# Optimization experiments

Measured on AMD Instinct MI355X. Metric: run time of the kernel, lower is better.

Reference implementation:

```python
import jax, jax.numpy as jnp
import numpy as np

# ---- static config (mirrors YOLOLayer init kwargs) ----
ANCHORS_ALL = jnp.array([[10.,13.],[16.,30.],[33.,23.],[30.,61.],[62.,45.],
                         [59.,119.],[116.,90.],[156.,198.],[373.,326.]], jnp.float32)
MASK = jnp.array([0, 1, 2], jnp.int32)
ANCHORS_PX = ANCHORS_ALL[:3]          # this scale's anchors, pixels
NUM_CLASSES = 1                       # forced by p_boxes.view(..., 6) in _first_loss
IMG_W = IMG_H = 608.0
B, A, GH, GW = 32, 3, 76, 76          # stride-8 head of a 608x608 YOLOv3
T = 48                                # number of ground-truth boxes
IGNORE_THRES = 0.5                    # ignore_thres_first_loss


def _bce(p, t):
    # torch BCELoss clamps log terms at -100
    return -(t * jnp.clip(jnp.log(p), -100.0) + (1.0 - t) * jnp.clip(jnp.log(1.0 - p), -100.0))


def _xywh2xyxy(b):
    xy, wh = b[..., :2], b[..., 2:4]
    return jnp.concatenate([xy - wh / 2, xy + wh / 2], -1)


def setup_inputs() -> dict:
    key = jax.random.key(0)
    k1, k2, k3 = jax.random.split(key, 3)
    x = jax.random.normal(k1, (B, A * (5 + NUM_CLASSES), GH, GW), jnp.float32) * 0.5
    # targets: [image_idx, cx, cy, w, h, cls], normalized coords; ids sorted, first = 0
    img_ids = jnp.sort(jnp.arange(T) % B).astype(jnp.float32)
    xy = jax.random.uniform(k2, (T, 2), minval=0.05, maxval=0.95)
    wh = jax.random.uniform(k3, (T, 2), minval=0.02, maxval=0.30)
    cls = jnp.zeros((T, 1), jnp.float32)
    target = jnp.concatenate([img_ids[:, None], xy, wh, cls], axis=1)
    return {"x": x, "target": target}


def _forward(x, target):
    stride_w, stride_h = IMG_W / GW, IMG_H / GH
    scale_anchors = ANCHORS_PX / jnp.array([stride_w, stride_h], jnp.float32)  # grid units

    pred = x.reshape(B, A, 5 + NUM_CLASSES, GH, GW).transpose(0, 1, 3, 4, 2)   # [B,A,H,W,5+C]
    cx = jax.nn.sigmoid(pred[..., 0]); cy = jax.nn.sigmoid(pred[..., 1])
    pw = pred[..., 2]; ph = pred[..., 3]
    pconf = jax.nn.sigmoid(pred[..., 4]); pcls = jax.nn.sigmoid(pred[..., 5:])

    # ---- __detect: decode boxes to pixel coords ----
    bx = cx + jnp.arange(GW, dtype=jnp.float32)[None, None, None, :]
    by = cy + jnp.arange(GH, dtype=jnp.float32)[None, None, :, None]
    bw = jnp.exp(pw) * scale_anchors[:, 0][None, :, None, None]
    bh = jnp.exp(ph) * scale_anchors[:, 1][None, :, None, None]
    boxes_px = jnp.stack([bx * stride_w, by * stride_h, bw * stride_w, bh * stride_h], -1).reshape(B, -1, 4)
    output = jnp.concatenate([boxes_px, pconf.reshape(B, -1, 1), pcls.reshape(B, -1, NUM_CLASSES)], -1)

    # ---- _first_loss: ignore mask from IoU(decoded preds, GT) in normalized coords ----
    timg = (target[:, 0] - target[0, 0]).astype(jnp.int32)                 # [T]
    tb = target[:, 1:5]                                                    # normalized xywh
    pbn = jnp.stack([bx / GW, by / GH, bw / GW, bh / GH], -1).reshape(B, -1, 4)  # [B,M,4]
    tc = _xywh2xyxy(tb)[:, None, None, :]                                  # [T,1,1,4]
    pc = _xywh2xyxy(pbn)[None]                                             # [1,B,M,4]
    iw = jnp.clip(jnp.minimum(tc[..., 2], pc[..., 2]) - jnp.maximum(tc[..., 0], pc[..., 0]), 0.0)
    ih = jnp.clip(jnp.minimum(tc[..., 3], pc[..., 3]) - jnp.maximum(tc[..., 1], pc[..., 1]), 0.0)
    inter = iw * ih
    ta = (tb[:, 2] * tb[:, 3])[:, None, None]
    pa = (pbn[..., 2] * pbn[..., 3])[None]
    iou = inter / (ta + pa - inter + 1e-16)                                # [T,B,M]
    match = timg[:, None] == jnp.arange(B)[None, :]                        # [T,B] GT-to-image
    best = jnp.max(jnp.where(match[:, :, None], iou, -1.0), 0)             # [B,M]
    ignore_mask = (best <= IGNORE_THRES).astype(jnp.float32).reshape(B, A, GH, GW)

    # ---- __build_target ----
    gxy = tb[:, :2] * jnp.array([GW, GH], jnp.float32)
    gwh = tb[:, 2:4] * jnp.array([GW, GH], jnp.float32)
    gwh_n = tb[:, 2:4]
    label = target[:, 5].astype(jnp.int32)
    an = ANCHORS_ALL / jnp.array([IMG_W, IMG_H], jnp.float32)              # [9,2] normalized
    w_inter = jnp.minimum(an[:, 0:1], gwh_n[None, :, 0]) * jnp.minimum(an[:, 1:2], gwh_n[None, :, 1])
    w_union = (an[:, 0] * an[:, 1] + 1e-16)[:, None] + (gwh_n[:, 0] * gwh_n[:, 1])[None, :] - w_inter
    anc_iou = w_inter / w_union                                            # [9,T]
    best_idx = jnp.argmax(anc_iou, 0)                                      # [T]
    gi = gxy[:, 0].astype(jnp.int32); gj = gxy[:, 1].astype(jnp.int32)
    in_mask = jnp.any(best_idx[:, None] == MASK[None, :], 1)
    valid = in_mask & (gi < GW) & (gj < GH) & (gi >= 0) & (gj >= 0)
    bi = best_idx - MASK[0]
    sc = 2.0 - gwh_n[:, 0] * gwh_n[:, 1]
    img_s = jnp.where(valid, timg, B)          # invalid rows -> OOB batch idx, dropped by scatter
    idx = (img_s, bi, gj, gi)

    z = jnp.zeros((B, A, GH, GW), jnp.float32)
    obj = z.at[idx].set(1.0, mode='drop')
    noobj = jnp.ones((B, A, GH, GW), jnp.float32).at[idx].set(0.0, mode='drop')
    tx = z.at[idx].set(gxy[:, 0] - jnp.floor(gxy[:, 0]), mode='drop')
    ty = z.at[idx].set(gxy[:, 1] - jnp.floor(gxy[:, 1]), mode='drop')
    tw = z.at[idx].set(jnp.log(gwh[:, 0] * stride_w / ANCHORS_PX[bi, 0] + 1e-16), mode='drop')
    th = z.at[idx].set(jnp.log(gwh[:, 1] * stride_h / ANCHORS_PX[bi, 1] + 1e-16), mode='drop')
    tconf = obj
    tcls = jnp.zeros((B, A, GH, GW, NUM_CLASSES), jnp.float32).at[img_s, bi, gj, gi, label].set(1.0, mode='drop')
    scale = jnp.ones((B, A, GH, GW), jnp.float32).at[idx].set(sc, mode='drop')

    # ignore_mask[obj==1] = 1 ; noobj_mask[ignore_mask==0] = 0
    ignore = jnp.where(obj > 0, 1.0, ignore_mask)
    noobj = jnp.where(ignore == 0, 0.0, noobj)

    s2 = scale * scale
    loss_x = jnp.sum(obj * (cx - tx) ** 2 * s2)
    loss_y = jnp.sum(obj * (cy - ty) ** 2 * s2)
    loss_w = jnp.sum(obj * (pw - tw) ** 2 * s2)
    loss_h = jnp.sum(obj * (ph - th) ** 2 * s2)
    loss_conf_obj = jnp.sum(obj * _bce(pconf, tconf))
    loss_conf_noobj = jnp.sum(noobj * _bce(pconf, tconf))
    loss_cls = jnp.sum(obj[..., None] * _bce(pcls, tcls))
    loss_conf = loss_conf_obj + loss_conf_noobj
    total = loss_x + loss_y + loss_w + loss_h + loss_conf + loss_cls
    r = lambda v: jnp.reshape(v, (1,))
    return (output, r(total), r(loss_x + loss_y), r(loss_w + loss_h), r(loss_conf), r(loss_cls))


def reference(x, target):
    return _forward(x, target)
```

## Files before the change

### kernel.cpp

```cpp
#include <hip/hip_runtime.h>

#define NB 32
#define NA 3
#define NGH 76
#define NGW 76
#define NT 48
#define PLANE (NGH * NGW)
#define NCELL (NB * NA * PLANE)
#define NOUT  (NCELL * 6)
#define CPT 2
#define BLK 256
#define NTHREAD (NCELL / CPT)
#define NBLKS (NTHREAD / BLK)
#define MAGIC 0x59A10C47u

static_assert(NTHREAD % BLK == 0, "grid must divide evenly");
static_assert(5 * BLK >= NBLKS, "poll covers all flags in one unrolled pass");


__launch_bounds__(BLK, 6)
__global__ void yolo_main(const float* __restrict__ x,
                          const float* __restrict__ tgt,
                          float* __restrict__ out,
                          float* __restrict__ partials,
                          unsigned int* __restrict__ flags,
                          float* __restrict__ lossbuf) {
    __shared__ float st[NT * 16];
    __shared__ unsigned long long sball[NB];
    __shared__ int soff[NB + 1];
    __shared__ int sord[NT];
    __shared__ float red[4][4];

    const int tx  = threadIdx.x;
    const int bid = blockIdx.x;
    const int tid = bid * BLK + tx;
    const int g   = tid * CPT;

    const int gw0 = g % NGW;
    const int gh  = (g / NGW) % NGH;
    const int a   = (g / PLANE) % NA;
    const int b   = g / (NA * PLANE);

    const float* xp = x + (size_t)(b * (NA * 6) + a * 6) * PLANE + (g % PLANE);
    const float2 v0 = *(const float2*)(xp);
    const float2 v1 = *(const float2*)(xp + PLANE);
    const float2 v2 = *(const float2*)(xp + 2 * PLANE);
    const float2 v3 = *(const float2*)(xp + 3 * PLANE);
    const float2 v4 = *(const float2*)(xp + 4 * PLANE);
    const float2 v5 = *(const float2*)(xp + 5 * PLANE);

    if (tx < 64) {
        const int t = tx;
        const bool isT = (t < NT);
        int timg = 999;
        if (isT) {
            const float t00 = tgt[0];
            const float* tr = tgt + t * 6;
            timg = (int)(tr[0] - t00);
            const float bxn = tr[1], byn = tr[2], bwn = tr[3], bhn = tr[4];

            const float gx = bxn * (float)NGW;
            const float gy = byn * (float)NGH;
            const int gi = (int)gx;
            const int gj = (int)gy;
            const float tarea = bwn * bhn;

            const float aw_px[9] = {10.f,16.f,33.f,30.f,62.f,59.f,116.f,156.f,373.f};
            const float ah_px[9] = {13.f,30.f,23.f,61.f,45.f,119.f,90.f,198.f,326.f};
            int bidx = 0; float biou = -1e30f;
            #pragma unroll
            for (int k = 0; k < 9; ++k) {
                const float aw = aw_px[k] / 608.0f;
                const float ah = ah_px[k] / 608.0f;
                const float wi = fminf(aw, bwn) * fminf(ah, bhn);
                const float un = ((aw * ah + 1e-16f) + tarea) - wi;
                const float iou = wi / un;
                if (iou > biou) { biou = iou; bidx = k; }
            }
            const bool inm = (bidx >= 0) && (bidx <= 2);
            const bool valid = inm && (gi < NGW) && (gj < NGH) && (gi >= 0) && (gj >= 0);
            const int bic = bidx < 0 ? 0 : (bidx > 2 ? 2 : bidx);
            const float apw = (bic == 0) ? 10.f : ((bic == 1) ? 16.f : 33.f);
            const float aph = (bic == 0) ? 13.f : ((bic == 1) ? 30.f : 23.f);

            float* s = st + t * 16;
            s[0]  = (float)timg;
            s[1]  = valid ? 1.0f : 0.0f;
            s[2]  = (float)bidx;
            s[3]  = (float)gj;
            s[4]  = (float)gi;
            s[5]  = gx - floorf(gx);
            s[6]  = gy - floorf(gy);
            s[7]  = __logf(((bwn * (float)NGW) * 8.0f) / apw + 1e-16f);
            s[8]  = __logf(((bhn * (float)NGH) * 8.0f) / aph + 1e-16f);
            s[9]  = 2.0f - bwn * bhn;
            s[10] = bxn - bwn * 0.5f;
            s[11] = byn - bhn * 0.5f;
            s[12] = bxn + bwn * 0.5f;
            s[13] = byn + bhn * 0.5f;
            s[14] = tarea;
            s[15] = 0.0f;
        }

        int cnt = 0;
        for (int bb = 0; bb < NB; ++bb) {
            const unsigned long long m = __ballot(timg == bb);
            if (t == 0) sball[bb] = m;
            if (t == bb) cnt = (int)__popcll(m);
        }
        int inc = cnt;
        #pragma unroll
        for (int d = 1; d < 32; d <<= 1) {
            const int v = __shfl_up(inc, d);
            if (t >= d) inc += v;
        }
        if (t < NB) soff[t] = inc - cnt;
        if (t == NB - 1) soff[NB] = inc;
        if (isT) {
            const unsigned long long m = sball[timg];
            const int rank = (int)__popcll(m & ((1ULL << t) - 1ULL));
            sord[soff[timg] + rank] = t;
        }
    }

    const float p0[CPT] = {v0.x, v0.y};
    const float p1[CPT] = {v1.x, v1.y};
    const float p2[CPT] = {v2.x, v2.y};
    const float p3[CPT] = {v3.x, v3.y};
    const float p4[CPT] = {v4.x, v4.y};
    const float p5[CPT] = {v5.x, v5.y};

    const float sa_w = (a == 0) ? 1.25f  : ((a == 1) ? 2.0f  : 4.125f);
    const float sa_h = (a == 0) ? 1.625f : ((a == 1) ? 3.75f : 2.875f);

    float cxv[CPT], cyv[CPT], pcf[CPT], pcl[CPT];
    float px1[CPT], py1[CPT], px2[CPT], py2[CPT], par[CPT];
    float o12[CPT * 6];

    #pragma unroll
    for (int c = 0; c < CPT; ++c) {
        const float cx    = 1.0f / (1.0f + __expf(-p0[c]));
        const float cy    = 1.0f / (1.0f + __expf(-p1[c]));
        const float pconf = 1.0f / (1.0f + __expf(-p4[c]));
        const float pcls  = 1.0f / (1.0f + __expf(-p5[c]));
        const float bx = cx + (float)(gw0 + c);
        const float by = cy + (float)gh;
        const float bw = __expf(p2[c]) * sa_w;
        const float bh = __expf(p3[c]) * sa_h;

        o12[c * 6 + 0] = bx * 8.0f;
        o12[c * 6 + 1] = by * 8.0f;
        o12[c * 6 + 2] = bw * 8.0f;
        o12[c * 6 + 3] = bh * 8.0f;
        o12[c * 6 + 4] = pconf;
        o12[c * 6 + 5] = pcls;

        const float pxc = bx * (1.0f / NGW), pyc = by * (1.0f / NGH);
        const float pwn = bw * (1.0f / NGW), phn = bh * (1.0f / NGH);
        cxv[c] = cx; cyv[c] = cy; pcf[c] = pconf; pcl[c] = pcls;
        px1[c] = pxc - pwn * 0.5f; py1[c] = pyc - phn * 0.5f;
        px2[c] = pxc + pwn * 0.5f; py2[c] = pyc + phn * 0.5f;
        par[c] = pwn * phn;
    }

    {
        float4* ob = (float4*)(out + (size_t)g * 6);
        ob[0] = make_float4(o12[0], o12[1], o12[2],  o12[3]);
        ob[1] = make_float4(o12[4], o12[5], o12[6],  o12[7]);
        ob[2] = make_float4(o12[8], o12[9], o12[10], o12[11]);
    }

    __syncthreads();

    float best[CPT] = {-1.f, -1.f};
    int   so[CPT]   = {-1, -1};
    {
        const int j1 = soff[b + 1];
        for (int j = soff[b]; j < j1; ++j) {
            const int t = sord[j];
            const float* s = st + t * 16;
            const float s1 = s[1], s2f = s[2], s3f = s[3], s4f = s[4];
            const float x1 = s[10], y1 = s[11], x2 = s[12], y2 = s[13], ta = s[14];
            const bool vmatch = (s1 != 0.0f) && ((int)s2f == a) && ((int)s3f == gh);
            #pragma unroll
            for (int c = 0; c < CPT; ++c) {
                const float iw = fmaxf(fminf(x2, px2[c]) - fmaxf(x1, px1[c]), 0.0f);
                const float ih = fmaxf(fminf(y2, py2[c]) - fmaxf(y1, py1[c]), 0.0f);
                const float inter = iw * ih;
                const float iou = inter / (((ta + par[c]) - inter) + 1e-16f);
                if (iou > best[c]) best[c] = iou;
                if (vmatch && ((int)s4f == gw0 + c)) so[c] = t;
            }
        }
    }

    float lxy = 0.f, lwh = 0.f, lconf = 0.f, lcls = 0.f;
    #pragma unroll
    for (int c = 0; c < CPT; ++c) {
        if (so[c] >= 0) {
            const float* s = st + so[c] * 16;
            const float sc = s[9], s2 = sc * sc;
            const float dx = cxv[c] - s[5], dy = cyv[c] - s[6];
            const float dw = p2[c] - s[7], dh = p3[c] - s[8];
            lxy   += (dx * dx + dy * dy) * s2;
            lwh   += (dw * dw + dh * dh) * s2;
            lconf += -fmaxf(__logf(pcf[c]), -100.0f);
            lcls  += -fmaxf(__logf(pcl[c]), -100.0f);
        } else if (best[c] <= 0.5f) {
            lconf += -fmaxf(__logf(1.0f - pcf[c]), -100.0f);
        }
    }

    #pragma unroll
    for (int off = 32; off > 0; off >>= 1) {
        lxy   += __shfl_down(lxy, off);
        lwh   += __shfl_down(lwh, off);
        lconf += __shfl_down(lconf, off);
        lcls  += __shfl_down(lcls, off);
    }
    const int lane = tx & 63, wv = tx >> 6;
    if (lane == 0) { red[wv][0] = lxy; red[wv][1] = lwh; red[wv][2] = lconf; red[wv][3] = lcls; }
    __syncthreads();
    if (tx == 0) {
        __hip_atomic_store(&partials[bid * 4 + 0], red[0][0] + red[1][0] + red[2][0] + red[3][0], __ATOMIC_RELAXED, __HIP_MEMORY_SCOPE_AGENT);
        __hip_atomic_store(&partials[bid * 4 + 1], red[0][1] + red[1][1] + red[2][1] + red[3][1], __ATOMIC_RELAXED, __HIP_MEMORY_SCOPE_AGENT);
        __hip_atomic_store(&partials[bid * 4 + 2], red[0][2] + red[1][2] + red[2][2] + red[3][2], __ATOMIC_RELAXED, __HIP_MEMORY_SCOPE_AGENT);
        __hip_atomic_store(&partials[bid * 4 + 3], red[0][3] + red[1][3] + red[2][3] + red[3][3], __ATOMIC_RELAXED, __HIP_MEMORY_SCOPE_AGENT);
        asm volatile("s_waitcnt vmcnt(0)" ::: "memory");
        __hip_atomic_store(&flags[bid], MAGIC, __ATOMIC_RELAXED, __HIP_MEMORY_SCOPE_AGENT);
    }

    if (bid == 0) {
        for (;;) {
            const unsigned f0 = __hip_atomic_load(&flags[tx], __ATOMIC_RELAXED, __HIP_MEMORY_SCOPE_AGENT);
            const unsigned f1 = __hip_atomic_load(&flags[tx + BLK], __ATOMIC_RELAXED, __HIP_MEMORY_SCOPE_AGENT);
            const unsigned f2 = __hip_atomic_load(&flags[tx + 2 * BLK], __ATOMIC_RELAXED, __HIP_MEMORY_SCOPE_AGENT);
            const unsigned f3 = __hip_atomic_load(&flags[tx + 3 * BLK], __ATOMIC_RELAXED, __HIP_MEMORY_SCOPE_AGENT);
            const unsigned f4_ = (tx + 4 * BLK < NBLKS)
                ? __hip_atomic_load(&flags[tx + 4 * BLK], __ATOMIC_RELAXED, __HIP_MEMORY_SCOPE_AGENT)
                : MAGIC;
            const int ok = (f0 == MAGIC) & (f1 == MAGIC) & (f2 == MAGIC) & (f3 == MAGIC) & (f4_ == MAGIC);
            if (__syncthreads_and(ok)) break;
            __builtin_amdgcn_s_sleep(16);
        }

        float a0 = 0.f, a1 = 0.f, a2 = 0.f, a3 = 0.f;
        #pragma unroll
        for (int k = 0; k < 5; ++k) {
            const int i = tx + k * BLK;
            if (i < NBLKS) {
                const float q0 = __hip_atomic_load(&partials[i * 4 + 0], __ATOMIC_RELAXED, __HIP_MEMORY_SCOPE_AGENT);
                const float q1 = __hip_atomic_load(&partials[i * 4 + 1], __ATOMIC_RELAXED, __HIP_MEMORY_SCOPE_AGENT);
                const float q2 = __hip_atomic_load(&partials[i * 4 + 2], __ATOMIC_RELAXED, __HIP_MEMORY_SCOPE_AGENT);
                const float q3 = __hip_atomic_load(&partials[i * 4 + 3], __ATOMIC_RELAXED, __HIP_MEMORY_SCOPE_AGENT);
                a0 += q0; a1 += q1; a2 += q2; a3 += q3;
            }
        }
        #pragma unroll
        for (int off = 32; off > 0; off >>= 1) {
            a0 += __shfl_down(a0, off);
            a1 += __shfl_down(a1, off);
            a2 += __shfl_down(a2, off);
            a3 += __shfl_down(a3, off);
        }
        if (lane == 0) { red[wv][0] = a0; red[wv][1] = a1; red[wv][2] = a2; red[wv][3] = a3; }
        __syncthreads();
        if (tx == 0) {
            const float s0 = red[0][0] + red[1][0] + red[2][0] + red[3][0];
            const float s1 = red[0][1] + red[1][1] + red[2][1] + red[3][1];
            const float s2 = red[0][2] + red[1][2] + red[2][2] + red[3][2];
            const float s3 = red[0][3] + red[1][3] + red[2][3] + red[3][3];
            lossbuf[1] = s0;
            lossbuf[2] = s1;
            lossbuf[3] = s2;
            lossbuf[4] = s3;
            lossbuf[0] = ((s0 + s1) + s2) + s3;
        }
    }
}

extern "C" void kernel_launch(void* const* d_in, const int* in_sizes, int n_in,
                              void* d_out, int out_size, void* d_ws, size_t ws_size,
                              hipStream_t stream) {
    const float* x   = (const float*)d_in[0];
    const float* tgt = (const float*)d_in[1];
    float* out          = (float*)d_out;
    float* lossbuf      = out + NOUT;
    float* partials     = (float*)d_ws;
    unsigned int* flags = (unsigned int*)(partials + NBLKS * 4);

    hipLaunchKernelGGL(yolo_main, dim3(NBLKS), dim3(BLK), 0, stream,
                       x, tgt, out, partials, flags, lossbuf);
    (void)in_sizes; (void)n_in; (void)out_size; (void)ws_size;
}
```

Measured before the change: 16.25 us.

## Build per-wavefront target tables to remove block-wide barrier before matching

Each of the four wavefronts now computes its own copy of the target table, per-image offsets and sorted order in shared memory. The only ordering left is a wave-local LDS wait, so the __syncthreads between the prologue and the matching loop goes away. This removes the stall where three waves waited on wave 0's target preprocessing, at the cost of four times the redundant setup work and shared memory. It also shortens the spin-wait sleep in the final reducer block and adds a barrier before the red array is reused.

```diff
diff --git a/kernel.cpp b/kernel.cpp
--- a/kernel.cpp
+++ b/kernel.cpp
@@ -25,14 +25,14 @@
                           float* __restrict__ partials,
                           unsigned int* __restrict__ flags,
                           float* __restrict__ lossbuf) {
-    __shared__ float st[NT * 16];
-    __shared__ unsigned long long sball[NB];
-    __shared__ int soff[NB + 1];
-    __shared__ int sord[NT];
+    __shared__ float st[4][NT * 16];
+    __shared__ int   soff[4][NB + 1];
+    __shared__ int   sord[4][NT];
     __shared__ float red[4][4];
 
     const int tx  = threadIdx.x;
     const int bid = blockIdx.x;
+    const int lane = tx & 63, wv = tx >> 6;
     const int tid = bid * BLK + tx;
     const int g   = tid * CPT;
 
@@ -49,8 +49,8 @@
     const float2 v4 = *(const float2*)(xp + 4 * PLANE);
     const float2 v5 = *(const float2*)(xp + 5 * PLANE);
 
-    if (tx < 64) {
-        const int t = tx;
+    {
+        const int t = lane;
         const bool isT = (t < NT);
         int timg = 999;
         if (isT) {
@@ -83,7 +83,7 @@
             const float apw = (bic == 0) ? 10.f : ((bic == 1) ? 16.f : 33.f);
             const float aph = (bic == 0) ? 13.f : ((bic == 1) ? 30.f : 23.f);
 
-            float* s = st + t * 16;
+            float* s = &st[wv][t * 16];
             s[0]  = (float)timg;
             s[1]  = valid ? 1.0f : 0.0f;
             s[2]  = (float)bidx;
@@ -102,11 +102,12 @@
             s[15] = 0.0f;
         }
 
+        unsigned long long mymask = 0ULL;
         int cnt = 0;
         for (int bb = 0; bb < NB; ++bb) {
             const unsigned long long m = __ballot(timg == bb);
-            if (t == 0) sball[bb] = m;
             if (t == bb) cnt = (int)__popcll(m);
+            if (timg == bb) mymask = m;
         }
         int inc = cnt;
         #pragma unroll
@@ -114,14 +115,18 @@
             const int v = __shfl_up(inc, d);
             if (t >= d) inc += v;
         }
-        if (t < NB) soff[t] = inc - cnt;
-        if (t == NB - 1) soff[NB] = inc;
+        if (t < NB) soff[wv][t] = inc - cnt;
+        if (t == NB - 1) soff[wv][NB] = inc;
         if (isT) {
-            const unsigned long long m = sball[timg];
-            const int rank = (int)__popcll(m & ((1ULL << t) - 1ULL));
-            sord[soff[timg] + rank] = t;
-        }
-    }
+            const int incT = __shfl(inc, timg);
+            const int cntT = __shfl(cnt, timg);
+            const int rank = (int)__popcll(mymask & ((1ULL << t) - 1ULL));
+            sord[wv][(incT - cntT) + rank] = t;
+        }
+    }
+    __builtin_amdgcn_sched_barrier(0);
+    asm volatile("s_waitcnt lgkmcnt(0)" ::: "memory");
+    __builtin_amdgcn_sched_barrier(0);
 
     const float p0[CPT] = {v0.x, v0.y};
     const float p1[CPT] = {v1.x, v1.y};
@@ -170,15 +175,13 @@
         ob[2] = make_float4(o12[8], o12[9], o12[10], o12[11]);
     }
 
-    __syncthreads();
-
     float best[CPT] = {-1.f, -1.f};
     int   so[CPT]   = {-1, -1};
     {
-        const int j1 = soff[b + 1];
-        for (int j = soff[b]; j < j1; ++j) {
-            const int t = sord[j];
-            const float* s = st + t * 16;
+        const int j1 = soff[wv][b + 1];
+        for (int j = soff[wv][b]; j < j1; ++j) {
+            const int t = sord[wv][j];
+            const float* s = &st[wv][t * 16];
             const float s1 = s[1], s2f = s[2], s3f = s[3], s4f = s[4];
             const float x1 = s[10], y1 = s[11], x2 = s[12], y2 = s[13], ta = s[14];
             const bool vmatch = (s1 != 0.0f) && ((int)s2f == a) && ((int)s3f == gh);
@@ -198,7 +201,7 @@
     #pragma unroll
     for (int c = 0; c < CPT; ++c) {
         if (so[c] >= 0) {
-            const float* s = st + so[c] * 16;
+            const float* s = &st[wv][so[c] * 16];
             const float sc = s[9], s2 = sc * sc;
             const float dx = cxv[c] - s[5], dy = cyv[c] - s[6];
             const float dw = p2[c] - s[7], dh = p3[c] - s[8];
@@ -218,7 +221,6 @@
         lconf += __shfl_down(lconf, off);
         lcls  += __shfl_down(lcls, off);
     }
-    const int lane = tx & 63, wv = tx >> 6;
     if (lane == 0) { red[wv][0] = lxy; red[wv][1] = lwh; red[wv][2] = lconf; red[wv][3] = lcls; }
     __syncthreads();
     if (tx == 0) {
@@ -241,7 +243,7 @@
                 : MAGIC;
             const int ok = (f0 == MAGIC) & (f1 == MAGIC) & (f2 == MAGIC) & (f3 == MAGIC) & (f4_ == MAGIC);
             if (__syncthreads_and(ok)) break;
-            __builtin_amdgcn_s_sleep(16);
+            __builtin_amdgcn_s_sleep(2);
         }
 
         float a0 = 0.f, a1 = 0.f, a2 = 0.f, a3 = 0.f;
@@ -263,6 +265,7 @@
             a2 += __shfl_down(a2, off);
             a3 += __shfl_down(a3, off);
         }
+        __syncthreads();
         if (lane == 0) { red[wv][0] = a0; red[wv][1] = a1; red[wv][2] = a2; red[wv][3] = a3; }
         __syncthreads();
         if (tx == 0) {
```

After: 17.34 us. +6.7%, slower.
